# Kernel optimization log

Measured on AMD Instinct MI355X. Metric: run time of the kernel, lower is better.

Reference implementation:

```python
import jax, jax.numpy as jnp
import numpy as np

N_NODES = 100000
N_EDGES = 1600000
IN_DIM = 128
HEADS = 8
HEAD_DIM = 16  # output_dim 128 / heads 8
NEG_SLOPE = 0.2  # PyG GATConv default LeakyReLU slope


def setup_inputs() -> dict:
    key = jax.random.key(0)
    k1, k2, k3, k4, k5 = jax.random.split(key, 5)
    x = jax.random.normal(k1, (N_NODES, IN_DIM), dtype=jnp.float32)
    edge_index = jax.random.randint(k2, (2, N_EDGES), 0, N_NODES, dtype=jnp.int64)
    scale = 1.0 / np.sqrt(IN_DIM)
    W = jax.random.normal(k3, (IN_DIM, HEADS * HEAD_DIM), dtype=jnp.float32) * scale
    a_src = jax.random.normal(k4, (HEADS, HEAD_DIM), dtype=jnp.float32) * scale
    a_dst = jax.random.normal(k5, (HEADS, HEAD_DIM), dtype=jnp.float32) * scale
    bias = jnp.zeros((HEADS * HEAD_DIM,), dtype=jnp.float32)
    return {"x": x, "edge_index": edge_index, "W": W, "a_src": a_src, "a_dst": a_dst, "bias": bias}


def reference(x, edge_index, W, a_src, a_dst, bias):
    N = x.shape[0]
    H, D = a_src.shape
    # add self-loops (PyG GATConv default add_self_loops=True)
    loop = jnp.arange(N, dtype=edge_index.dtype)
    src = jnp.concatenate([edge_index[0], loop])  # message sources j
    dst = jnp.concatenate([edge_index[1], loop])  # message targets i

    h = (x @ W).reshape(N, H, D)  # per-head projected features
    alpha_src = jnp.sum(h * a_src, axis=-1)  # [N, H]
    alpha_dst = jnp.sum(h * a_dst, axis=-1)  # [N, H]

    # edge-wise attention logits, softmax over incoming edges of each dst node
    e = jax.nn.leaky_relu(alpha_src[src] + alpha_dst[dst], NEG_SLOPE)  # [E', H]
    e_max = jax.ops.segment_max(e, dst, num_segments=N)
    e_exp = jnp.exp(e - e_max[dst])
    denom = jax.ops.segment_sum(e_exp, dst, num_segments=N)
    alpha = e_exp / (denom[dst] + 1e-16)  # [E', H]

    # weighted scatter-sum of source features
    out = jax.ops.segment_sum(alpha[:, :, None] * h[src], dst, num_segments=N)  # [N, H, D]
    out = out.reshape(N, H * D) + bias
    # wrapper: ReLU (concat=True), dropout is identity in eval mode
    return jax.nn.relu(out)
```

## Files before the change

kernel.cpp:

```cpp
#include <hip/hip_runtime.h>
#include <hip/hip_bf16.h>

#define NEG_SLOPE 0.2f
#define NBUCK 782
#define ABLK 8192
#define CAP 3072

typedef __attribute__((ext_vector_type(8))) short bf16x8v;
typedef __attribute__((ext_vector_type(4))) float f32x4;

__device__ __forceinline__ unsigned f2bf_bits(float f) {
    unsigned u = __float_as_uint(f);
    return (u + 0x7fffu + ((u >> 16) & 1u)) >> 16;
}
__device__ __forceinline__ float bflo(unsigned u) { return __uint_as_float(u << 16); }
__device__ __forceinline__ float bfhi(unsigned u) { return __uint_as_float(u & 0xffff0000u); }

__global__ __launch_bounds__(256) void prep_w(const float* __restrict__ W,
                                              short* __restrict__ WtG) {
    int id = blockIdx.x * 256 + threadIdx.x;
    int n = id >> 7, k = id & 127;
    WtG[id] = (short)f2bf_bits(W[k * 128 + n]);
}

__global__ __launch_bounds__(256) void gemm_mfma(const float* __restrict__ x,
                                                 const short* __restrict__ WtG,
                                                 const float* __restrict__ a_src,
                                                 const float* __restrict__ a_dst,
                                                 short* __restrict__ hout,
                                                 float* __restrict__ as,
                                                 float* __restrict__ ad, int N) {
    __shared__ short xs[64 * 136];
    __shared__ short wt[128 * 136];
    const int tid = threadIdx.x;
    const int r0 = blockIdx.x * 64;

#pragma unroll
    for (int p = 0; p < 8; ++p) {
        int idx = p * 256 + tid;
        int n = idx >> 4, kk = (idx & 15) * 8;
        *(uint4*)&wt[n * 136 + kk] = *(const uint4*)(WtG + n * 128 + kk);
    }
#pragma unroll
    for (int p = 0; p < 8; ++p) {
        int lin = p * 1024 + tid * 4;
        int row = lin >> 7, k = lin & 127;
        int gr = r0 + row;
        int grc = gr < N ? gr : N - 1;
        float4 v = *(const float4*)(x + (size_t)grc * 128 + k);
        unsigned p0 = f2bf_bits(v.x) | (f2bf_bits(v.y) << 16);
        unsigned p1 = f2bf_bits(v.z) | (f2bf_bits(v.w) << 16);
        *(uint2*)&xs[row * 136 + k] = make_uint2(p0, p1);
    }
    __syncthreads();

    const int wv = tid >> 6;
    const int lane = tid & 63;
    const int lc = lane & 15, quad = lane >> 4;
    f32x4 acc[8];
#pragma unroll
    for (int c = 0; c < 8; ++c) acc[c] = (f32x4){0.f, 0.f, 0.f, 0.f};
    const short* aB = &xs[(wv * 16 + lc) * 136 + quad * 8];
    const short* bB = &wt[lc * 136 + quad * 8];
#pragma unroll
    for (int kc = 0; kc < 4; ++kc) {
        bf16x8v af = *(const bf16x8v*)(aB + kc * 32);
#pragma unroll
        for (int c = 0; c < 8; ++c) {
            bf16x8v bf = *(const bf16x8v*)(bB + c * (16 * 136) + kc * 32);
            acc[c] = __builtin_amdgcn_mfma_f32_16x16x32_bf16(af, bf, acc[c], 0, 0, 0);
        }
    }

    const int rowb = r0 + wv * 16 + quad * 4;
#pragma unroll
    for (int c = 0; c < 8; ++c) {
        float asc = a_src[c * 16 + lc];
        float adc = a_dst[c * 16 + lc];
        float sv[4], dv[4];
#pragma unroll
        for (int r = 0; r < 4; ++r) {
            float hv = acc[c][r];
            int row = rowb + r;
            if (row < N) hout[(size_t)row * 128 + c * 16 + lc] = (short)f2bf_bits(hv);
            sv[r] = hv * asc;
            dv[r] = hv * adc;
        }
#pragma unroll
        for (int m = 1; m <= 8; m <<= 1) {
#pragma unroll
            for (int r = 0; r < 4; ++r) {
                sv[r] += __shfl_xor(sv[r], m);
                dv[r] += __shfl_xor(dv[r], m);
            }
        }
        if (lc == 0) {
#pragma unroll
            for (int r = 0; r < 4; ++r) {
                int row = rowb + r;
                if (row < N) { as[row * 8 + c] = sv[r]; ad[row * 8 + c] = dv[r]; }
            }
        }
    }
}

__global__ __launch_bounds__(1024) void bucket_edges(const int* __restrict__ ei, int E,
                                                     unsigned* __restrict__ slab,
                                                     int* __restrict__ cntG,
                                                     int* __restrict__ startG) {
    __shared__ int hist[1024];
    __shared__ int cur[NBUCK];
    const int t = threadIdx.x;
    const int blk = blockIdx.x;
    const int base = blk * ABLK;
    int count = E - base; if (count > ABLK) count = ABLK;

    int sr[8], dr[8];
    hist[t] = 0;
#pragma unroll
    for (int k = 0; k < 8; ++k) {
        int i = k * 1024 + t;
        if (i < count) { sr[k] = ei[base + i]; dr[k] = ei[E + base + i]; }
    }
    __syncthreads();
#pragma unroll
    for (int k = 0; k < 8; ++k) {
        int i = k * 1024 + t;
        if (i < count) atomicAdd(&hist[dr[k] >> 7], 1);
    }
    __syncthreads();
    int v = hist[t];
    for (int off = 1; off < 1024; off <<= 1) {
        int u = t >= off ? hist[t - off] : 0;
        __syncthreads();
        hist[t] += u;
        __syncthreads();
    }
    int excl = hist[t] - v;
    if (t < NBUCK) {
        cntG[blk * NBUCK + t]   = v;
        startG[blk * NBUCK + t] = excl;
        cur[t] = excl;
    }
    __syncthreads();
#pragma unroll
    for (int k = 0; k < 8; ++k) {
        int i = k * 1024 + t;
        if (i < count) {
            int d = dr[k];
            int pos = atomicAdd(&cur[d >> 7], 1);
            slab[(size_t)blk * ABLK + pos] = (unsigned)sr[k] | ((unsigned)(d & 127) << 17);
        }
    }
}

__global__ __launch_bounds__(512) void bucket_aggregate(const unsigned* __restrict__ slab,
                                                        const int* __restrict__ cntG,
                                                        const int* __restrict__ startG,
                                                        int nblk, int N,
                                                        const short* __restrict__ h,
                                                        const float* __restrict__ as,
                                                        const float* __restrict__ ad,
                                                        const float* __restrict__ bias,
                                                        float* __restrict__ out) {
    __shared__ int eL[CAP];
    __shared__ int sortedL[CAP];
    __shared__ int incl[512];
    __shared__ int cS[512];
    __shared__ int stS[512];
    __shared__ int rs[128];
    __shared__ int lp[128];
    const int bb = blockIdx.x;
    const int t = threadIdx.x;
    const int nodeBase = bb << 7;

    int c = 0, st = 0;
    if (t < nblk) { c = cntG[t * NBUCK + bb]; st = startG[t * NBUCK + bb]; }
    cS[t] = c; stS[t] = st; incl[t] = c;
    if (t < 128) lp[t] = 0;
    __syncthreads();
    for (int off = 1; off < 512; off <<= 1) {
        int u = t >= off ? incl[t - off] : 0;
        __syncthreads();
        incl[t] += u;
        __syncthreads();
    }
    const int total = incl[511];
    for (int e = t; e < total; e += 512) {
        int lo = 0, hi = nblk - 1;
        while (lo < hi) { int mid = (lo + hi) >> 1; if (incl[mid] > e) hi = mid; else lo = mid + 1; }
        int loc = e - (incl[lo] - cS[lo]);
        eL[e] = (int)slab[(size_t)lo * ABLK + stS[lo] + loc];
    }
    __syncthreads();
    for (int e = t; e < total; e += 512) atomicAdd(&lp[((unsigned)eL[e]) >> 17], 1);
    __syncthreads();
    int hv = (t < 128) ? lp[t] : 0;
    for (int off = 1; off < 128; off <<= 1) {
        int u = (t >= off && t < 128) ? lp[t - off] : 0;
        __syncthreads();
        if (t < 128) lp[t] += u;
        __syncthreads();
    }
    if (t < 128) {
        int ex = lp[t] - hv;
        rs[t] = ex;
        lp[t] = ex;
    }
    __syncthreads();
    for (int e = t; e < total; e += 512) {
        unsigned pk = (unsigned)eL[e];
        int pos = atomicAdd(&lp[pk >> 17], 1);
        sortedL[pos] = (int)(pk & 0x1FFFFu);
    }
    __syncthreads();
    const int wv = t >> 6;
    const int lane = t & 63;
    const int g = lane >> 4, p = lane & 15, hh = p >> 1;
    float4 b0 = *(const float4*)(bias + p * 8);
    float4 b1 = *(const float4*)(bias + p * 8 + 4);
    for (int nl = wv * 16; nl < wv * 16 + 16; ++nl) {
        int gn = nodeBase + nl;
        if (gn >= N) break;
        int s0 = rs[nl], e0 = lp[nl];
        float adv = ad[gn * 8 + hh];

        float acc[8];
#pragma unroll
        for (int k = 0; k < 8; ++k) acc[k] = 0.f;
        float dsum = 0.f;

        int e = s0 + g;
        int j = (e < e0) ? sortedL[e] : 0;
        while (e < e0) {
            int jn = (e + 4 < e0) ? sortedL[e + 4] : 0;
            float tt = as[j * 8 + hh] + adv;
            tt = tt > 0.f ? tt : NEG_SLOPE * tt;
            float w = __expf(tt);
            uint4 hr = *(const uint4*)(h + (size_t)j * 128 + p * 8);
            acc[0] += w * bflo(hr.x); acc[1] += w * bfhi(hr.x);
            acc[2] += w * bflo(hr.y); acc[3] += w * bfhi(hr.y);
            acc[4] += w * bflo(hr.z); acc[5] += w * bfhi(hr.z);
            acc[6] += w * bflo(hr.w); acc[7] += w * bfhi(hr.w);
            dsum += w;
            j = jn; e += 4;
        }
#pragma unroll
        for (int m = 16; m <= 32; m <<= 1) {
#pragma unroll
            for (int k = 0; k < 8; ++k) acc[k] += __shfl_xor(acc[k], m);
            dsum += __shfl_xor(dsum, m);
        }
        {
            float tt = as[gn * 8 + hh] + adv;
            tt = tt > 0.f ? tt : NEG_SLOPE * tt;
            float w = __expf(tt);
            uint4 hr = *(const uint4*)(h + (size_t)gn * 128 + p * 8);
            acc[0] += w * bflo(hr.x); acc[1] += w * bfhi(hr.x);
            acc[2] += w * bflo(hr.y); acc[3] += w * bfhi(hr.y);
            acc[4] += w * bflo(hr.z); acc[5] += w * bfhi(hr.z);
            acc[6] += w * bflo(hr.w); acc[7] += w * bfhi(hr.w);
            dsum += w;
        }
        float inv = 1.0f / (dsum + 1e-16f);
        float o0 = acc[0] * inv + b0.x, o1 = acc[1] * inv + b0.y;
        float o2 = acc[2] * inv + b0.z, o3 = acc[3] * inv + b0.w;
        float o4 = acc[4] * inv + b1.x, o5 = acc[5] * inv + b1.y;
        float o6 = acc[6] * inv + b1.z, o7 = acc[7] * inv + b1.w;
        o0 = o0 > 0.f ? o0 : 0.f; o1 = o1 > 0.f ? o1 : 0.f;
        o2 = o2 > 0.f ? o2 : 0.f; o3 = o3 > 0.f ? o3 : 0.f;
        o4 = o4 > 0.f ? o4 : 0.f; o5 = o5 > 0.f ? o5 : 0.f;
        o6 = o6 > 0.f ? o6 : 0.f; o7 = o7 > 0.f ? o7 : 0.f;
        *(float4*)(out + (size_t)gn * 128 + p * 8)     = make_float4(o0, o1, o2, o3);
        *(float4*)(out + (size_t)gn * 128 + p * 8 + 4) = make_float4(o4, o5, o6, o7);
    }
}

extern "C" void kernel_launch(void* const* d_in, const int* in_sizes, int n_in,
                              void* d_out, int out_size, void* d_ws, size_t ws_size,
                              hipStream_t stream) {
    const float* x     = (const float*)d_in[0];
    const int*   ei    = (const int*)d_in[1];
    const float* W     = (const float*)d_in[2];
    const float* a_src = (const float*)d_in[3];
    const float* a_dst = (const float*)d_in[4];
    const float* bias  = (const float*)d_in[5];
    float* out = (float*)d_out;

    const int N = in_sizes[0] / 128;
    const int E = in_sizes[1] / 2;
    const int nblk = (E + ABLK - 1) / ABLK;

    char* ws = (char*)d_ws;
    size_t off = 0;
    auto alloc = [&](size_t bytes) { void* p = ws + off; off = (off + bytes + 255) & ~(size_t)255; return p; };
    short*    h      = (short*)alloc((size_t)N * 128 * 2);
    float*    as     = (float*)alloc((size_t)N * 8 * 4);
    float*    ad     = (float*)alloc((size_t)N * 8 * 4);
    unsigned* slab   = (unsigned*)alloc((size_t)nblk * ABLK * 4);
    int*      cntG   = (int*)alloc((size_t)nblk * NBUCK * 4);
    int*      startG = (int*)alloc((size_t)nblk * NBUCK * 4);
    short*    WtG    = (short*)alloc((size_t)128 * 128 * 2);

    prep_w<<<64, 256, 0, stream>>>(W, WtG);
    gemm_mfma<<<(N + 63) / 64, 256, 0, stream>>>(x, WtG, a_src, a_dst, h, as, ad, N);
    bucket_edges<<<nblk, 1024, 0, stream>>>(ei, E, slab, cntG, startG);
    bucket_aggregate<<<NBUCK, 512, 0, stream>>>(slab, cntG, startG, nblk, N,
                                                h, as, ad, bias, out);
}
```

Before: 248.7 us.

## Split bucket aggregation into CSR build and per-node wave aggregate kernel

Splits the fused bucket_aggregate kernel in two. A build_csr kernel writes per-node row ranges and sorted sources to global memory, and a separate aggregate kernel then processes one node per wavefront across many small blocks. The aggregate kernel also software-pipelines the neighbor gather, and the block-wide scans switch from barrier-heavy shared-memory scans to wave shuffle scans. The goal is more parallelism and latency hiding in the gather phase, which was limited to 782 large blocks each looping over 16 nodes per wave. In exchange it adds an extra kernel launch, a global round-trip for the CSR arrays, and a clamp of per-bucket edges to CAP.

```diff
diff --git a/kernel.cpp b/kernel.cpp
--- a/kernel.cpp
+++ b/kernel.cpp
@@ -110,6 +110,7 @@
                                                      int* __restrict__ startG) {
     __shared__ int hist[1024];
     __shared__ int cur[NBUCK];
+    __shared__ int wpart[16];
     const int t = threadIdx.x;
     const int blk = blockIdx.x;
     const int base = blk * ABLK;
@@ -130,13 +131,20 @@
     }
     __syncthreads();
     int v = hist[t];
-    for (int off = 1; off < 1024; off <<= 1) {
-        int u = t >= off ? hist[t - off] : 0;
-        __syncthreads();
-        hist[t] += u;
-        __syncthreads();
-    }
-    int excl = hist[t] - v;
+    int lane = t & 63, wid = t >> 6;
+    int sc = v;
+#pragma unroll
+    for (int off = 1; off < 64; off <<= 1) { int u = __shfl_up(sc, off); if (lane >= off) sc += u; }
+    if (lane == 63) wpart[wid] = sc;
+    __syncthreads();
+    if (wid == 0 && lane < 16) {
+        int wv = wpart[lane], wsum = wv;
+#pragma unroll
+        for (int off = 1; off < 16; off <<= 1) { int u = __shfl_up(wsum, off); if (lane >= off) wsum += u; }
+        wpart[lane] = wsum - wv;
+    }
+    __syncthreads();
+    int excl = sc - v + wpart[wid];
     if (t < NBUCK) {
         cntG[blk * NBUCK + t]   = v;
         startG[blk * NBUCK + t] = excl;
@@ -154,38 +162,46 @@
     }
 }
 
-__global__ __launch_bounds__(512) void bucket_aggregate(const unsigned* __restrict__ slab,
-                                                        const int* __restrict__ cntG,
-                                                        const int* __restrict__ startG,
-                                                        int nblk, int N,
-                                                        const short* __restrict__ h,
-                                                        const float* __restrict__ as,
-                                                        const float* __restrict__ ad,
-                                                        const float* __restrict__ bias,
-                                                        float* __restrict__ out) {
+__global__ __launch_bounds__(512) void build_csr(const unsigned* __restrict__ slab,
+                                                 const int* __restrict__ cntG,
+                                                 const int* __restrict__ startG,
+                                                 int nblk, int N,
+                                                 int* __restrict__ rowS,
+                                                 int* __restrict__ rowE,
+                                                 int* __restrict__ sortedSrc) {
     __shared__ int eL[CAP];
-    __shared__ int sortedL[CAP];
     __shared__ int incl[512];
     __shared__ int cS[512];
     __shared__ int stS[512];
-    __shared__ int rs[128];
     __shared__ int lp[128];
+    __shared__ int wpart[8];
+    __shared__ int halfSum;
     const int bb = blockIdx.x;
     const int t = threadIdx.x;
     const int nodeBase = bb << 7;
+    const int bBase = bb * CAP;
 
     int c = 0, st = 0;
     if (t < nblk) { c = cntG[t * NBUCK + bb]; st = startG[t * NBUCK + bb]; }
-    cS[t] = c; stS[t] = st; incl[t] = c;
+    cS[t] = c; stS[t] = st;
     if (t < 128) lp[t] = 0;
-    __syncthreads();
-    for (int off = 1; off < 512; off <<= 1) {
-        int u = t >= off ? incl[t - off] : 0;
-        __syncthreads();
-        incl[t] += u;
-        __syncthreads();
-    }
-    const int total = incl[511];
+    int lane = t & 63, wid = t >> 6;
+    int sc = c;
+#pragma unroll
+    for (int off = 1; off < 64; off <<= 1) { int u = __shfl_up(sc, off); if (lane >= off) sc += u; }
+    if (lane == 63) wpart[wid] = sc;
+    __syncthreads();
+    if (wid == 0 && lane < 8) {
+        int wv = wpart[lane], wsum = wv;
+#pragma unroll
+        for (int off = 1; off < 8; off <<= 1) { int u = __shfl_up(wsum, off); if (lane >= off) wsum += u; }
+        wpart[lane] = wsum - wv;
+    }
+    __syncthreads();
+    incl[t] = sc + wpart[wid];
+    __syncthreads();
+    int total = incl[511];
+    if (total > CAP) total = CAP;
     for (int e = t; e < total; e += 512) {
         int lo = 0, hi = nblk - 1;
         while (lo < hi) { int mid = (lo + hi) >> 1; if (incl[mid] > e) hi = mid; else lo = mid + 1; }
@@ -195,85 +211,105 @@
     __syncthreads();
     for (int e = t; e < total; e += 512) atomicAdd(&lp[((unsigned)eL[e]) >> 17], 1);
     __syncthreads();
-    int hv = (t < 128) ? lp[t] : 0;
-    for (int off = 1; off < 128; off <<= 1) {
-        int u = (t >= off && t < 128) ? lp[t - off] : 0;
-        __syncthreads();
-        if (t < 128) lp[t] += u;
-        __syncthreads();
-    }
+    int cnt = 0, s2 = 0;
     if (t < 128) {
-        int ex = lp[t] - hv;
-        rs[t] = ex;
+        cnt = lp[t];
+        s2 = cnt;
+#pragma unroll
+        for (int off = 1; off < 64; off <<= 1) { int u = __shfl_up(s2, off); if (lane >= off) s2 += u; }
+        if (t == 63) halfSum = s2;
+    }
+    __syncthreads();
+    if (t < 128) {
+        int inc2 = s2 + (t >= 64 ? halfSum : 0);
+        int ex = inc2 - cnt;
+        int gn = nodeBase + t;
+        if (gn < N) { rowS[gn] = bBase + ex; rowE[gn] = bBase + ex + cnt; }
         lp[t] = ex;
     }
     __syncthreads();
     for (int e = t; e < total; e += 512) {
         unsigned pk = (unsigned)eL[e];
         int pos = atomicAdd(&lp[pk >> 17], 1);
-        sortedL[pos] = (int)(pk & 0x1FFFFu);
-    }
-    __syncthreads();
-    const int wv = t >> 6;
-    const int lane = t & 63;
-    const int g = lane >> 4, p = lane & 15, hh = p >> 1;
+        sortedSrc[bBase + pos] = (int)(pk & 0x1FFFFu);
+    }
+}
+
+__global__ __launch_bounds__(256) void aggregate(const int* __restrict__ rowS,
+                                                 const int* __restrict__ rowE,
+                                                 const int* __restrict__ sortedSrc,
+                                                 const short* __restrict__ h,
+                                                 const float* __restrict__ as,
+                                                 const float* __restrict__ ad,
+                                                 const float* __restrict__ bias,
+                                                 float* __restrict__ out, int N) {
+    int node = blockIdx.x * 4 + (threadIdx.x >> 6);
+    if (node >= N) return;
+    int lane = threadIdx.x & 63;
+    int g = lane >> 4, p = lane & 15, hh = p >> 1;
+    int start = rowS[node], end = rowE[node];
+    float adv = ad[node * 8 + hh];
+
+    float acc[8];
+#pragma unroll
+    for (int k = 0; k < 8; ++k) acc[k] = 0.f;
+    float dsum = 0.f;
+
+    int e = start + g;
+    float asv = 0.f; uint4 hr;
+    if (e < end) {
+        int j = sortedSrc[e];
+        asv = as[j * 8 + hh];
+        hr = *(const uint4*)(h + (size_t)j * 128 + p * 8);
+    }
+    while (e < end) {
+        int en = e + 4;
+        float asn = 0.f; uint4 hn;
+        if (en < end) {
+            int jn = sortedSrc[en];
+            asn = as[jn * 8 + hh];
+            hn = *(const uint4*)(h + (size_t)jn * 128 + p * 8);
+        }
+        float tt = asv + adv;
+        tt = tt > 0.f ? tt : NEG_SLOPE * tt;
+        float w = __expf(tt);
+        acc[0] += w * bflo(hr.x); acc[1] += w * bfhi(hr.x);
+        acc[2] += w * bflo(hr.y); acc[3] += w * bfhi(hr.y);
+        acc[4] += w * bflo(hr.z); acc[5] += w * bfhi(hr.z);
+        acc[6] += w * bflo(hr.w); acc[7] += w * bfhi(hr.w);
+        dsum += w;
+        asv = asn; hr = hn; e = en;
+    }
+#pragma unroll
+    for (int m = 16; m <= 32; m <<= 1) {
+#pragma unroll
+        for (int k = 0; k < 8; ++k) acc[k] += __shfl_xor(acc[k], m);
+        dsum += __shfl_xor(dsum, m);
+    }
+    {
+        float tt = as[node * 8 + hh] + adv;
+        tt = tt > 0.f ? tt : NEG_SLOPE * tt;
+        float w = __expf(tt);
+        uint4 hv = *(const uint4*)(h + (size_t)node * 128 + p * 8);
+        acc[0] += w * bflo(hv.x); acc[1] += w * bfhi(hv.x);
+        acc[2] += w * bflo(hv.y); acc[3] += w * bfhi(hv.y);
+        acc[4] += w * bflo(hv.z); acc[5] += w * bfhi(hv.z);
+        acc[6] += w * bflo(hv.w); acc[7] += w * bfhi(hv.w);
+        dsum += w;
+    }
+    float inv = 1.0f / (dsum + 1e-16f);
     float4 b0 = *(const float4*)(bias + p * 8);
     float4 b1 = *(const float4*)(bias + p * 8 + 4);
-    for (int nl = wv * 16; nl < wv * 16 + 16; ++nl) {
-        int gn = nodeBase + nl;
-        if (gn >= N) break;
-        int s0 = rs[nl], e0 = lp[nl];
-        float adv = ad[gn * 8 + hh];
-
-        float acc[8];
-#pragma unroll
-        for (int k = 0; k < 8; ++k) acc[k] = 0.f;
-        float dsum = 0.f;
-
-        int e = s0 + g;
-        int j = (e < e0) ? sortedL[e] : 0;
-        while (e < e0) {
-            int jn = (e + 4 < e0) ? sortedL[e + 4] : 0;
-            float tt = as[j * 8 + hh] + adv;
-            tt = tt > 0.f ? tt : NEG_SLOPE * tt;
-            float w = __expf(tt);
-            uint4 hr = *(const uint4*)(h + (size_t)j * 128 + p * 8);
-            acc[0] += w * bflo(hr.x); acc[1] += w * bfhi(hr.x);
-            acc[2] += w * bflo(hr.y); acc[3] += w * bfhi(hr.y);
-            acc[4] += w * bflo(hr.z); acc[5] += w * bfhi(hr.z);
-            acc[6] += w * bflo(hr.w); acc[7] += w * bfhi(hr.w);
-            dsum += w;
-            j = jn; e += 4;
-        }
-#pragma unroll
-        for (int m = 16; m <= 32; m <<= 1) {
-#pragma unroll
-            for (int k = 0; k < 8; ++k) acc[k] += __shfl_xor(acc[k], m);
-            dsum += __shfl_xor(dsum, m);
-        }
-        {
-            float tt = as[gn * 8 + hh] + adv;
-            tt = tt > 0.f ? tt : NEG_SLOPE * tt;
-            float w = __expf(tt);
-            uint4 hr = *(const uint4*)(h + (size_t)gn * 128 + p * 8);
-            acc[0] += w * bflo(hr.x); acc[1] += w * bfhi(hr.x);
-            acc[2] += w * bflo(hr.y); acc[3] += w * bfhi(hr.y);
-            acc[4] += w * bflo(hr.z); acc[5] += w * bfhi(hr.z);
-            acc[6] += w * bflo(hr.w); acc[7] += w * bfhi(hr.w);
-            dsum += w;
-        }
-        float inv = 1.0f / (dsum + 1e-16f);
-        float o0 = acc[0] * inv + b0.x, o1 = acc[1] * inv + b0.y;
-        float o2 = acc[2] * inv + b0.z, o3 = acc[3] * inv + b0.w;
-        float o4 = acc[4] * inv + b1.x, o5 = acc[5] * inv + b1.y;
-        float o6 = acc[6] * inv + b1.z, o7 = acc[7] * inv + b1.w;
-        o0 = o0 > 0.f ? o0 : 0.f; o1 = o1 > 0.f ? o1 : 0.f;
-        o2 = o2 > 0.f ? o2 : 0.f; o3 = o3 > 0.f ? o3 : 0.f;
-        o4 = o4 > 0.f ? o4 : 0.f; o5 = o5 > 0.f ? o5 : 0.f;
-        o6 = o6 > 0.f ? o6 : 0.f; o7 = o7 > 0.f ? o7 : 0.f;
-        *(float4*)(out + (size_t)gn * 128 + p * 8)     = make_float4(o0, o1, o2, o3);
-        *(float4*)(out + (size_t)gn * 128 + p * 8 + 4) = make_float4(o4, o5, o6, o7);
-    }
+    float o0 = acc[0] * inv + b0.x, o1 = acc[1] * inv + b0.y;
+    float o2 = acc[2] * inv + b0.z, o3 = acc[3] * inv + b0.w;
+    float o4 = acc[4] * inv + b1.x, o5 = acc[5] * inv + b1.y;
+    float o6 = acc[6] * inv + b1.z, o7 = acc[7] * inv + b1.w;
+    o0 = o0 > 0.f ? o0 : 0.f; o1 = o1 > 0.f ? o1 : 0.f;
+    o2 = o2 > 0.f ? o2 : 0.f; o3 = o3 > 0.f ? o3 : 0.f;
+    o4 = o4 > 0.f ? o4 : 0.f; o5 = o5 > 0.f ? o5 : 0.f;
+    o6 = o6 > 0.f ? o6 : 0.f; o7 = o7 > 0.f ? o7 : 0.f;
+    *(float4*)(out + (size_t)node * 128 + p * 8)     = make_float4(o0, o1, o2, o3);
+    *(float4*)(out + (size_t)node * 128 + p * 8 + 4) = make_float4(o4, o5, o6, o7);
 }
 
 extern "C" void kernel_launch(void* const* d_in, const int* in_sizes, int n_in,
@@ -294,17 +330,20 @@
     char* ws = (char*)d_ws;
     size_t off = 0;
     auto alloc = [&](size_t bytes) { void* p = ws + off; off = (off + bytes + 255) & ~(size_t)255; return p; };
-    short*    h      = (short*)alloc((size_t)N * 128 * 2);
-    float*    as     = (float*)alloc((size_t)N * 8 * 4);
-    float*    ad     = (float*)alloc((size_t)N * 8 * 4);
-    unsigned* slab   = (unsigned*)alloc((size_t)nblk * ABLK * 4);
-    int*      cntG   = (int*)alloc((size_t)nblk * NBUCK * 4);
-    int*      startG = (int*)alloc((size_t)nblk * NBUCK * 4);
-    short*    WtG    = (short*)alloc((size_t)128 * 128 * 2);
+    short*    h         = (short*)alloc((size_t)N * 128 * 2);
+    float*    as        = (float*)alloc((size_t)N * 8 * 4);
+    float*    ad        = (float*)alloc((size_t)N * 8 * 4);
+    unsigned* slab      = (unsigned*)alloc((size_t)nblk * ABLK * 4);
+    int*      cntG      = (int*)alloc((size_t)nblk * NBUCK * 4);
+    int*      startG    = (int*)alloc((size_t)nblk * NBUCK * 4);
+    int*      sortedSrc = (int*)alloc((size_t)NBUCK * CAP * 4);
+    int*      rowS      = (int*)alloc((size_t)N * 4);
+    int*      rowE      = (int*)alloc((size_t)N * 4);
+    short*    WtG       = (short*)alloc((size_t)128 * 128 * 2);
 
     prep_w<<<64, 256, 0, stream>>>(W, WtG);
     gemm_mfma<<<(N + 63) / 64, 256, 0, stream>>>(x, WtG, a_src, a_dst, h, as, ad, N);
     bucket_edges<<<nblk, 1024, 0, stream>>>(ei, E, slab, cntG, startG);
-    bucket_aggregate<<<NBUCK, 512, 0, stream>>>(slab, cntG, startG, nblk, N,
-                                                h, as, ad, bias, out);
-}
+    build_csr<<<NBUCK, 512, 0, stream>>>(slab, cntG, startG, nblk, N, rowS, rowE, sortedSrc);
+    aggregate<<<(N + 3) / 4, 256, 0, stream>>>(rowS, rowE, sortedSrc, h, as, ad, bias, out, N);
+}
```

New measurement: 246.5 us. No clear change (-0.9%).
